# Kernel optimization log

Hardware: AMD Instinct MI355X
Metric: run time of the kernel (lower is better)

The kernel has to match this reference:

```python
import jax, jax.numpy as jnp
import numpy as np

N_NODES = 100000
N_EDGES = 1600000
D_IN = 128
D_OUT = 128


def setup_inputs() -> dict:
    key = jax.random.key(0)
    k1, k2, k3, k4, k5 = jax.random.split(key, 5)
    x = jax.random.normal(k1, (N_NODES, D_IN), dtype=jnp.float32)
    edge_src = jax.random.randint(k2, (N_EDGES,), 0, N_NODES)
    edge_dst = jax.random.randint(k3, (N_EDGES,), 0, N_NODES)
    edge_weight = jax.random.uniform(k4, (N_EDGES,), dtype=jnp.float32)
    # xavier_normal_ std = sqrt(2 / (fan_in + fan_out))
    std = float(np.sqrt(2.0 / (D_IN + D_OUT)))
    W = jax.random.normal(k5, (D_IN, D_OUT), dtype=jnp.float32) * std
    bias = jnp.zeros((D_OUT,), dtype=jnp.float32)
    return {"x": x, "edge_src": edge_src, "edge_dst": edge_dst,
            "edge_weight": edge_weight, "W": W, "bias": bias}


def reference(x, edge_src, edge_dst, edge_weight, W, bias):
    # support = x @ W  (dense projection)
    support = x @ W  # [N, D_OUT]
    # out = adj @ support  (SpMM over COO edge list: out[dst] += w * support[src])
    msgs = edge_weight[:, None] * support[edge_src]  # [E, D_OUT]
    out = jax.ops.segment_sum(msgs, edge_dst, num_segments=N_NODES)
    return out + bias
```

## Files before the change

kernel.cpp:

```cpp
#include <hip/hip_runtime.h>

#define N_NODES 100000
#define N_EDGES 1600000
#define D 128
#define BM 64
#define LDK 136
#define LINK_BLOCKS (N_EDGES / 256)
#define GEMM_BLOCKS ((N_NODES + BM - 1) / BM)

using frag_ab = __attribute__((ext_vector_type(8))) short;
using f32x4  = __attribute__((ext_vector_type(4))) float;

__device__ __forceinline__ unsigned short f2bf(float f) {
  union { float f; unsigned int u; } a;
  a.f = f;
  unsigned int u = a.u;
  u += 0x7fffu + ((u >> 16) & 1u);
  return (unsigned short)(u >> 16);
}

__global__ __launch_bounds__(256) void link_gemm_kernel(
    const int* __restrict__ esrc, const int* __restrict__ edst,
    const float* __restrict__ ew, int* __restrict__ head,
    int2* __restrict__ node, const float* __restrict__ x,
    const float* __restrict__ W, unsigned short* __restrict__ support) {
  __shared__ unsigned short As[BM * LDK];
  __shared__ unsigned short Bs[128 * LDK];

  if (blockIdx.x < LINK_BLOCKS) {
    const int e = blockIdx.x * 256 + threadIdx.x;
    const int s = esrc[e];
    const int d = edst[e];
    const float w = ew[e];
    int w15 = (int)(w * 32768.0f);
    if (w15 > 32767) w15 = 32767;
    const int prev = atomicExch(&head[d], e);
    node[e] = make_int2((int)(((unsigned int)s << 15) | (unsigned int)w15), prev);
    return;
  }

  const int bid = blockIdx.x - LINK_BLOCKS;
  const int tid = threadIdx.x;
  const long r0 = (long)bid * BM;
  const int rows_here = (N_NODES - (int)r0 < BM) ? (N_NODES - (int)r0) : BM;

  const float4* x4 = reinterpret_cast<const float4*>(x) + r0 * 32;
#pragma unroll
  for (int i = 0; i < 8; ++i) {
    const int f = tid + i * 256;
    const int row = f >> 5, k4 = f & 31;
    float4 v = make_float4(0.f, 0.f, 0.f, 0.f);
    if (row < rows_here) v = x4[f];
    ushort4 h;
    h.x = f2bf(v.x); h.y = f2bf(v.y); h.z = f2bf(v.z); h.w = f2bf(v.w);
    *reinterpret_cast<ushort4*>(&As[row * LDK + k4 * 4]) = h;
  }

  const float4* W4 = reinterpret_cast<const float4*>(W);
#pragma unroll
  for (int i = 0; i < 16; ++i) {
    const int f = tid + i * 256;
    const int k = f >> 5, n4 = f & 31;
    const float4 v = W4[f];
    Bs[(n4 * 4 + 0) * LDK + k] = f2bf(v.x);
    Bs[(n4 * 4 + 1) * LDK + k] = f2bf(v.y);
    Bs[(n4 * 4 + 2) * LDK + k] = f2bf(v.z);
    Bs[(n4 * 4 + 3) * LDK + k] = f2bf(v.w);
  }

  __syncthreads();

  const int wid = tid >> 6;
  const int lane = tid & 63;
  const int lrow = lane & 15;
  const int kg = lane >> 4;

  f32x4 acc[8] = {};
#pragma unroll
  for (int ks = 0; ks < 4; ++ks) {
    const frag_ab a = *reinterpret_cast<const frag_ab*>(
        &As[(wid * 16 + lrow) * LDK + ks * 32 + kg * 8]);
#pragma unroll
    for (int cf = 0; cf < 8; ++cf) {
      const frag_ab b = *reinterpret_cast<const frag_ab*>(
          &Bs[(cf * 16 + lrow) * LDK + ks * 32 + kg * 8]);
      acc[cf] = __builtin_amdgcn_mfma_f32_16x16x32_bf16(a, b, acc[cf], 0, 0, 0);
    }
  }

  const int rbase = wid * 16 + (lane >> 4) * 4;
#pragma unroll
  for (int j = 0; j < 4; ++j) {
    const int row = rbase + j;
    if (row < rows_here) {
      unsigned short* orow = support + (r0 + row) * D;
#pragma unroll
      for (int cf = 0; cf < 8; ++cf) orow[cf * 16 + lrow] = f2bf(acc[cf][j]);
    }
  }
}

__global__ __launch_bounds__(256) void gather_ll_kernel(
    const uint4* __restrict__ sup4, const int* __restrict__ head,
    const int2* __restrict__ node, const float* __restrict__ bias,
    float* __restrict__ out) {
  const int wave = threadIdx.x >> 6;
  const int lane = threadIdx.x & 63;
  const int chain = lane >> 4;
  const int sub = lane & 15;
  const int nid = blockIdx.x * 16 + wave * 4 + chain;

  int e = head[nid];
  float a0 = 0.f, a1 = 0.f, a2 = 0.f, a3 = 0.f;
  float a4 = 0.f, a5 = 0.f, a6 = 0.f, a7 = 0.f;

  while ((unsigned int)e < (unsigned int)N_EDGES) {
    const int2 rec = node[e];
    const float w = (float)(rec.x & 0x7fff) * (1.0f / 32768.0f);
    const int src = (int)(((unsigned int)rec.x) >> 15);
    const uint4 v = sup4[(size_t)src * 16 + sub];
    a0 += w * __uint_as_float(v.x << 16);
    a1 += w * __uint_as_float(v.x & 0xffff0000u);
    a2 += w * __uint_as_float(v.y << 16);
    a3 += w * __uint_as_float(v.y & 0xffff0000u);
    a4 += w * __uint_as_float(v.z << 16);
    a5 += w * __uint_as_float(v.z & 0xffff0000u);
    a6 += w * __uint_as_float(v.w << 16);
    a7 += w * __uint_as_float(v.w & 0xffff0000u);
    e = rec.y;
  }

  const float4 b0 = reinterpret_cast<const float4*>(bias)[sub * 2 + 0];
  const float4 b1 = reinterpret_cast<const float4*>(bias)[sub * 2 + 1];
  float4* op = reinterpret_cast<float4*>(out + (size_t)nid * D);
  op[sub * 2 + 0] = make_float4(a0 + b0.x, a1 + b0.y, a2 + b0.z, a3 + b0.w);
  op[sub * 2 + 1] = make_float4(a4 + b1.x, a5 + b1.y, a6 + b1.z, a7 + b1.w);
}

extern "C" void kernel_launch(void* const* d_in, const int* in_sizes, int n_in,
                              void* d_out, int out_size, void* d_ws, size_t ws_size,
                              hipStream_t stream) {
  const float* x    = (const float*)d_in[0];
  const int*   esrc = (const int*)d_in[1];
  const int*   edst = (const int*)d_in[2];
  const float* ew   = (const float*)d_in[3];
  const float* W    = (const float*)d_in[4];
  const float* bias = (const float*)d_in[5];
  float* out = (float*)d_out;

  char* ws = (char*)d_ws;
  size_t off = 0;
  auto alloc = [&](size_t bytes) {
    void* p = ws + off;
    off += (bytes + 511) & ~(size_t)511;
    return p;
  };
  unsigned short* support = (unsigned short*)alloc((size_t)N_NODES * D * 2);
  int*  head = (int*)alloc((size_t)N_NODES * 4);
  int2* node = (int2*)alloc((size_t)N_EDGES * 8);

  link_gemm_kernel<<<LINK_BLOCKS + GEMM_BLOCKS, 256, 0, stream>>>(
      esrc, edst, ew, head, node, x, W, support);

  gather_ll_kernel<<<N_NODES / 16, 256, 0, stream>>>(
      (const uint4*)support, head, node, bias, out);
}
```

Baseline: 294.4 us.

## Pre-transpose W to bf16 once and load GEMM fragments directly from global memory

Adds a small kernel that converts W to a transposed bf16 copy once per call. The GEMM blocks then drop shared-memory staging and the block barrier, reading A fragments straight from x in global memory (converting to bf16 in registers) and B fragments from the cached transposed weights. This removes each block's redundant W conversion, the strided shared-memory stores and the 52KB of LDS, which should raise occupancy next to the link blocks. In exchange there is one extra kernel launch and more global/L2 traffic, since every wave re-reads W fragments from cache.

```diff
diff --git a/kernel.cpp b/kernel.cpp
--- a/kernel.cpp
+++ b/kernel.cpp
@@ -4,7 +4,6 @@
 #define N_EDGES 1600000
 #define D 128
 #define BM 64
-#define LDK 136
 #define LINK_BLOCKS (N_EDGES / 256)
 #define GEMM_BLOCKS ((N_NODES + BM - 1) / BM)
 
@@ -19,14 +18,19 @@
   return (unsigned short)(u >> 16);
 }
 
+__global__ __launch_bounds__(256) void wt_kernel(
+    const float* __restrict__ W, unsigned short* __restrict__ wT) {
+  const int flat = blockIdx.x * 256 + threadIdx.x;
+  const int n = flat >> 7, k = flat & 127;
+  wT[flat] = f2bf(W[k * 128 + n]);
+}
+
 __global__ __launch_bounds__(256) void link_gemm_kernel(
     const int* __restrict__ esrc, const int* __restrict__ edst,
     const float* __restrict__ ew, int* __restrict__ head,
     int2* __restrict__ node, const float* __restrict__ x,
-    const float* __restrict__ W, unsigned short* __restrict__ support) {
-  __shared__ unsigned short As[BM * LDK];
-  __shared__ unsigned short Bs[128 * LDK];
-
+    const unsigned short* __restrict__ wT,
+    unsigned short* __restrict__ support) {
   if (blockIdx.x < LINK_BLOCKS) {
     const int e = blockIdx.x * 256 + threadIdx.x;
     const int s = esrc[e];
@@ -41,59 +45,42 @@
 
   const int bid = blockIdx.x - LINK_BLOCKS;
   const int tid = threadIdx.x;
-  const long r0 = (long)bid * BM;
-  const int rows_here = (N_NODES - (int)r0 < BM) ? (N_NODES - (int)r0) : BM;
-
-  const float4* x4 = reinterpret_cast<const float4*>(x) + r0 * 32;
-#pragma unroll
-  for (int i = 0; i < 8; ++i) {
-    const int f = tid + i * 256;
-    const int row = f >> 5, k4 = f & 31;
-    float4 v = make_float4(0.f, 0.f, 0.f, 0.f);
-    if (row < rows_here) v = x4[f];
-    ushort4 h;
-    h.x = f2bf(v.x); h.y = f2bf(v.y); h.z = f2bf(v.z); h.w = f2bf(v.w);
-    *reinterpret_cast<ushort4*>(&As[row * LDK + k4 * 4]) = h;
-  }
-
-  const float4* W4 = reinterpret_cast<const float4*>(W);
-#pragma unroll
-  for (int i = 0; i < 16; ++i) {
-    const int f = tid + i * 256;
-    const int k = f >> 5, n4 = f & 31;
-    const float4 v = W4[f];
-    Bs[(n4 * 4 + 0) * LDK + k] = f2bf(v.x);
-    Bs[(n4 * 4 + 1) * LDK + k] = f2bf(v.y);
-    Bs[(n4 * 4 + 2) * LDK + k] = f2bf(v.z);
-    Bs[(n4 * 4 + 3) * LDK + k] = f2bf(v.w);
-  }
-
-  __syncthreads();
-
   const int wid = tid >> 6;
   const int lane = tid & 63;
   const int lrow = lane & 15;
   const int kg = lane >> 4;
 
+  const int grow = bid * BM + wid * 16 + lrow;
+  const bool rok = (grow < N_NODES);
+
   f32x4 acc[8] = {};
 #pragma unroll
   for (int ks = 0; ks < 4; ++ks) {
-    const frag_ab a = *reinterpret_cast<const frag_ab*>(
-        &As[(wid * 16 + lrow) * LDK + ks * 32 + kg * 8]);
+    frag_ab a = {};
+    if (rok) {
+      const float4* xr =
+          reinterpret_cast<const float4*>(x + (size_t)grow * D + ks * 32 + kg * 8);
+      const float4 p0 = xr[0];
+      const float4 p1 = xr[1];
+      a[0] = (short)f2bf(p0.x); a[1] = (short)f2bf(p0.y);
+      a[2] = (short)f2bf(p0.z); a[3] = (short)f2bf(p0.w);
+      a[4] = (short)f2bf(p1.x); a[5] = (short)f2bf(p1.y);
+      a[6] = (short)f2bf(p1.z); a[7] = (short)f2bf(p1.w);
+    }
 #pragma unroll
     for (int cf = 0; cf < 8; ++cf) {
       const frag_ab b = *reinterpret_cast<const frag_ab*>(
-          &Bs[(cf * 16 + lrow) * LDK + ks * 32 + kg * 8]);
+          &wT[(size_t)(cf * 16 + lrow) * D + ks * 32 + kg * 8]);
       acc[cf] = __builtin_amdgcn_mfma_f32_16x16x32_bf16(a, b, acc[cf], 0, 0, 0);
     }
   }
 
-  const int rbase = wid * 16 + (lane >> 4) * 4;
+  const int rbase = bid * BM + wid * 16 + (lane >> 4) * 4;
 #pragma unroll
   for (int j = 0; j < 4; ++j) {
     const int row = rbase + j;
-    if (row < rows_here) {
-      unsigned short* orow = support + (r0 + row) * D;
+    if (row < N_NODES) {
+      unsigned short* orow = support + (size_t)row * D;
 #pragma unroll
       for (int cf = 0; cf < 8; ++cf) orow[cf * 16 + lrow] = f2bf(acc[cf][j]);
     }
@@ -158,9 +145,12 @@
   unsigned short* support = (unsigned short*)alloc((size_t)N_NODES * D * 2);
   int*  head = (int*)alloc((size_t)N_NODES * 4);
   int2* node = (int2*)alloc((size_t)N_EDGES * 8);
+  unsigned short* wT = (unsigned short*)alloc((size_t)D * D * 2);
+
+  wt_kernel<<<64, 256, 0, stream>>>(W, wT);
 
   link_gemm_kernel<<<LINK_BLOCKS + GEMM_BLOCKS, 256, 0, stream>>>(
-      esrc, edst, ew, head, node, x, W, support);
+      esrc, edst, ew, head, node, x, wT, support);
 
   gather_ll_kernel<<<N_NODES / 16, 256, 0, stream>>>(
       (const uint4*)support, head, node, bias, out);
```

New measurement: 303.4 us. 1.03x slower.
